# Optimization experiments

Hardware: AMD Instinct MI355X
Metric: run time of the kernel (lower is better)

Reference implementation:

```python
import jax, jax.numpy as jnp
import numpy as np
from jax import lax

NIC = 3            # image channels (immutable)
NC = 20            # total channels
FIRE_RATE = 0.5


def _sobel_kernel(nc):
    # depthwise kernel OIHW: for each channel, [sobel_x, sobel_y]
    sx = jnp.array([[-1., 0., 1.], [-2., 0., 2.], [-1., 0., 1.]], jnp.float32) / 8.0
    sy = sx.T
    k = jnp.stack([sx, sy], 0)[None]              # [1, 2, 3, 3]
    k = jnp.tile(k, (nc, 1, 1, 1)).reshape(2 * nc, 1, 3, 3)
    return k


def _perceive(x, sobel_k):
    # reflect padding as in filter_padding='reflect'
    xp = jnp.pad(x, ((0, 0), (0, 0), (1, 1), (1, 1)), mode='reflect')
    grad = lax.conv_general_dilated(
        xp, sobel_k, window_strides=(1, 1), padding='VALID',
        dimension_numbers=('NCHW', 'OIHW', 'NCHW'),
        feature_group_count=x.shape[1])
    # identity + 2 filters -> [B, 3*NC, H, W]
    return jnp.concatenate([x, grad], axis=1)


def reference(x, W1, b1, W2, steps):
    B, C, H, W = x.shape
    sobel_k = _sobel_kernel(C)
    # mask that zeroes dx on immutable image channels
    chan_mask = jnp.concatenate([jnp.zeros((NIC,), x.dtype),
                                 jnp.ones((C - NIC,), x.dtype)])[None, :, None, None]
    base_key = jax.random.key(42)

    def step_fn(xc, step):
        p = _perceive(xc, sobel_k)                                  # [B,3C,H,W]
        h = jax.nn.relu(jnp.einsum('bchw,kc->bkhw', p, W1) + b1[None, :, None, None])
        dx = jnp.einsum('bkhw,ck->bchw', h, W2)                      # [B,C,H,W]
        key = jax.random.fold_in(base_key, step)
        S = (jax.random.uniform(key, (B, 1, H, W)) < FIRE_RATE).astype(xc.dtype)
        dx = dx * S * chan_mask
        return xc + dx, None

    x, _ = lax.scan(step_fn, x, jnp.arange(steps))
    return x


def setup_inputs() -> dict:
    key = jax.random.key(0)
    k1, k2, k3 = jax.random.split(key, 3)
    x = jax.random.normal(k1, (8, NC, 256, 256), jnp.float32)
    W1 = jax.random.normal(k2, (128, 3 * NC), jnp.float32) * (1.0 / np.sqrt(3 * NC))
    b1 = jnp.zeros((128,), jnp.float32)
    # last layer is near-zero initialized in NCA practice; keep small for stability over 64 steps
    W2 = jax.random.normal(k3, (NC, 128), jnp.float32) * 0.01
    return {"x": x, "W1": W1, "b1": b1, "W2": W2, "steps": 64}
```

## Files before the change

kernel.cpp:

```cpp
#include <hip/hip_runtime.h>
#include <stdint.h>
#include <stddef.h>

#define HH 256
#define WW 256
#define NCH 20
#define KH 128

__host__ __device__ inline void tf2x32(uint32_t k0, uint32_t k1,
                                       uint32_t x0, uint32_t x1,
                                       uint32_t* o0, uint32_t* o1) {
  uint32_t ks0 = k0, ks1 = k1, ks2 = k0 ^ k1 ^ 0x1BD11BDAu;
  x0 += ks0; x1 += ks1;
#define RND(r) { x0 += x1; x1 = (x1 << (r)) | (x1 >> (32 - (r))); x1 ^= x0; }
  RND(13) RND(15) RND(26) RND(6)   x0 += ks1; x1 += ks2 + 1u;
  RND(17) RND(29) RND(16) RND(24)  x0 += ks2; x1 += ks0 + 2u;
  RND(13) RND(15) RND(26) RND(6)   x0 += ks0; x1 += ks1 + 3u;
  RND(17) RND(29) RND(16) RND(24)  x0 += ks1; x1 += ks2 + 4u;
  RND(13) RND(15) RND(26) RND(6)   x0 += ks2; x1 += ks0 + 5u;
#undef RND
  *o0 = x0; *o1 = x1;
}

__global__ __launch_bounds__(256) void nca_step(
    const float* __restrict__ xin, float* __restrict__ xout,
    const float* __restrict__ W1, const float* __restrict__ b1,
    const float* __restrict__ W2, uint32_t fk0, uint32_t fk1)
{
  __shared__ float xs[NCH][18][18];

  const int tid = threadIdx.x;
  const int bx = blockIdx.x, by = blockIdx.y, bb = blockIdx.z;
  const int x0t = bx << 4, y0t = by << 4;
  const float* xb = xin + (size_t)bb * (NCH * HH * WW);

  for (int idx = tid; idx < NCH * 18 * 18; idx += 256) {
    int c  = idx / 324;
    int r  = idx - c * 324;
    int ly = r / 18;
    int lx = r - ly * 18;
    int gy = y0t + ly - 1;
    int gx = x0t + lx - 1;
    gy = (gy < 0) ? -gy : gy;  gy = (gy >= HH) ? (2 * HH - 2 - gy) : gy;
    gx = (gx < 0) ? -gx : gx;  gx = (gx >= WW) ? (2 * WW - 2 - gx) : gx;
    xs[c][ly][lx] = xb[c * (HH * WW) + gy * WW + gx];
  }
  __syncthreads();

  const int tx = tid & 15, ty = tid >> 4;

  float p[3 * NCH];
#pragma unroll
  for (int c = 0; c < NCH; ++c) {
    float a00 = xs[c][ty    ][tx    ], a01 = xs[c][ty    ][tx + 1], a02 = xs[c][ty    ][tx + 2];
    float a10 = xs[c][ty + 1][tx    ], a11 = xs[c][ty + 1][tx + 1], a12 = xs[c][ty + 1][tx + 2];
    float a20 = xs[c][ty + 2][tx    ], a21 = xs[c][ty + 2][tx + 1], a22 = xs[c][ty + 2][tx + 2];
    p[c] = a11;
    p[NCH + 2 * c    ] = ((a02 - a00) + 2.f * (a12 - a10) + (a22 - a20)) * 0.125f;
    p[NCH + 2 * c + 1] = ((a20 - a00) + 2.f * (a21 - a01) + (a22 - a02)) * 0.125f;
  }

  float dxv[NCH];
#pragma unroll
  for (int c = 0; c < NCH; ++c) dxv[c] = 0.f;

  for (int k = 0; k < KH; ++k) {
    const float* w1r = W1 + k * 60;
    float h0 = b1[k], h1 = 0.f, h2 = 0.f, h3 = 0.f;
#pragma unroll
    for (int c = 0; c < 60; c += 4) {
      h0 = fmaf(w1r[c    ], p[c    ], h0);
      h1 = fmaf(w1r[c + 1], p[c + 1], h1);
      h2 = fmaf(w1r[c + 2], p[c + 2], h2);
      h3 = fmaf(w1r[c + 3], p[c + 3], h3);
    }
    float hk = fmaxf((h0 + h1) + (h2 + h3), 0.f);
#pragma unroll
    for (int c = 0; c < NCH; ++c)
      dxv[c] = fmaf(W2[c * KH + k], hk, dxv[c]);
  }

  uint32_t f = ((uint32_t)bb << 16) | ((uint32_t)(y0t + ty) << 8) | (uint32_t)(x0t + tx);
  uint32_t o0, o1;
  tf2x32(fk0, fk1, 0u, f, &o0, &o1);
  uint32_t bits = o0 ^ o1;
  float u = __uint_as_float((bits >> 9) | 0x3f800000u) - 1.0f;
  float fire = (u < 0.5f) ? 1.0f : 0.0f;

  size_t obase = (size_t)bb * (NCH * HH * WW) + (size_t)(y0t + ty) * WW + (x0t + tx);
#pragma unroll
  for (int c = 0; c < NCH; ++c) {
    float v = p[c];
    if (c >= 3) v = v + dxv[c] * fire;
    xout[obase + c * (HH * WW)] = v;
  }
}

extern "C" void kernel_launch(void* const* d_in, const int* in_sizes, int n_in,
                              void* d_out, int out_size, void* d_ws, size_t ws_size,
                              hipStream_t stream) {
  const float* x  = (const float*)d_in[0];
  const float* W1 = (const float*)d_in[1];
  const float* b1 = (const float*)d_in[2];
  const float* W2 = (const float*)d_in[3];
  const int steps = 64;

  float* bufWs  = (float*)d_ws;
  float* bufOut = (float*)d_out;

  dim3 grid(WW / 16, HH / 16, 8);
  dim3 block(256);

  const float* src = x;
  for (int s = 0; s < steps; ++s) {
    uint32_t fk0, fk1;
    tf2x32(0u, 42u, 0u, (uint32_t)s, &fk0, &fk1);
    float* dst = ((steps - 1 - s) & 1) ? bufWs : bufOut;
    nca_step<<<grid, block, 0, stream>>>(src, dst, W1, b1, W2, fk0, fk1);
    src = dst;
  }
}
```

Before: 13.24 ms.

## Compute two vertically adjacent pixels per thread and stage W2/b1 in LDS

Each thread now handles two vertically adjacent pixels on a 16x32 tile, so every W1 weight load feeds two sets of FMAs and the halo overhead per pixel shrinks. W2 and b1 are copied into shared memory once per block and read as float4 vectors, and the k loop is kept rolled. The goal is to cut the scalar and global weight-load traffic per FMA in this compute-bound MLP. In exchange, register use roughly doubles and the launch bound asks for 2 blocks per CU, which could force spills, and the grid has half as many blocks.

```diff
diff --git a/kernel.cpp b/kernel.cpp
--- a/kernel.cpp
+++ b/kernel.cpp
@@ -6,6 +6,10 @@
 #define WW 256
 #define NCH 20
 #define KH 128
+#define TSX 16
+#define TSY 32
+#define HALO_W 18
+#define HALO_H 34
 
 __host__ __device__ inline void tf2x32(uint32_t k0, uint32_t k1,
                                        uint32_t x0, uint32_t x1,
@@ -22,77 +26,114 @@
   *o0 = x0; *o1 = x1;
 }
 
-__global__ __launch_bounds__(256) void nca_step(
+__device__ inline float fire_of(uint32_t fk0, uint32_t fk1, uint32_t f) {
+  uint32_t o0, o1;
+  tf2x32(fk0, fk1, 0u, f, &o0, &o1);
+  uint32_t bits = o0 ^ o1;
+  float u = __uint_as_float((bits >> 9) | 0x3f800000u) - 1.0f;
+  return (u < 0.5f) ? 1.0f : 0.0f;
+}
+
+__global__ __launch_bounds__(256, 2) void nca_step(
     const float* __restrict__ xin, float* __restrict__ xout,
     const float* __restrict__ W1, const float* __restrict__ b1,
     const float* __restrict__ W2, uint32_t fk0, uint32_t fk1)
 {
-  __shared__ float xs[NCH][18][18];
+  __shared__ float xs[NCH][HALO_H][HALO_W];
+  __shared__ float w2b[KH][24];
 
   const int tid = threadIdx.x;
   const int bx = blockIdx.x, by = blockIdx.y, bb = blockIdx.z;
-  const int x0t = bx << 4, y0t = by << 4;
+  const int x0t = bx * TSX, y0t = by * TSY;
   const float* xb = xin + (size_t)bb * (NCH * HH * WW);
 
-  for (int idx = tid; idx < NCH * 18 * 18; idx += 256) {
-    int c  = idx / 324;
-    int r  = idx - c * 324;
-    int ly = r / 18;
-    int lx = r - ly * 18;
+  for (int idx = tid; idx < NCH * HALO_H * HALO_W; idx += 256) {
+    int c  = idx / (HALO_H * HALO_W);
+    int r  = idx - c * (HALO_H * HALO_W);
+    int ly = r / HALO_W;
+    int lx = r - ly * HALO_W;
     int gy = y0t + ly - 1;
     int gx = x0t + lx - 1;
     gy = (gy < 0) ? -gy : gy;  gy = (gy >= HH) ? (2 * HH - 2 - gy) : gy;
     gx = (gx < 0) ? -gx : gx;  gx = (gx >= WW) ? (2 * WW - 2 - gx) : gx;
     xs[c][ly][lx] = xb[c * (HH * WW) + gy * WW + gx];
   }
+  for (int idx = tid; idx < KH * 21; idx += 256) {
+    int k = idx / 21, c = idx - k * 21;
+    w2b[k][c] = (c < 20) ? W2[c * KH + k] : b1[k];
+  }
   __syncthreads();
 
-  const int tx = tid & 15, ty = tid >> 4;
+  const int tx = tid & 15, tyy = tid >> 4;
+  const int r0 = 2 * tyy;
 
-  float p[3 * NCH];
+  float pA[60], pB[60];
 #pragma unroll
   for (int c = 0; c < NCH; ++c) {
-    float a00 = xs[c][ty    ][tx    ], a01 = xs[c][ty    ][tx + 1], a02 = xs[c][ty    ][tx + 2];
-    float a10 = xs[c][ty + 1][tx    ], a11 = xs[c][ty + 1][tx + 1], a12 = xs[c][ty + 1][tx + 2];
-    float a20 = xs[c][ty + 2][tx    ], a21 = xs[c][ty + 2][tx + 1], a22 = xs[c][ty + 2][tx + 2];
-    p[c] = a11;
-    p[NCH + 2 * c    ] = ((a02 - a00) + 2.f * (a12 - a10) + (a22 - a20)) * 0.125f;
-    p[NCH + 2 * c + 1] = ((a20 - a00) + 2.f * (a21 - a01) + (a22 - a02)) * 0.125f;
+    float t00 = xs[c][r0    ][tx], t01 = xs[c][r0    ][tx + 1], t02 = xs[c][r0    ][tx + 2];
+    float t10 = xs[c][r0 + 1][tx], t11 = xs[c][r0 + 1][tx + 1], t12 = xs[c][r0 + 1][tx + 2];
+    float t20 = xs[c][r0 + 2][tx], t21 = xs[c][r0 + 2][tx + 1], t22 = xs[c][r0 + 2][tx + 2];
+    float t30 = xs[c][r0 + 3][tx], t31 = xs[c][r0 + 3][tx + 1], t32 = xs[c][r0 + 3][tx + 2];
+    pA[c] = t11;
+    pB[c] = t21;
+    pA[NCH + 2 * c    ] = ((t02 - t00) + 2.f * (t12 - t10) + (t22 - t20)) * 0.125f;
+    pA[NCH + 2 * c + 1] = ((t20 - t00) + 2.f * (t21 - t01) + (t22 - t02)) * 0.125f;
+    pB[NCH + 2 * c    ] = ((t12 - t10) + 2.f * (t22 - t20) + (t32 - t30)) * 0.125f;
+    pB[NCH + 2 * c + 1] = ((t30 - t10) + 2.f * (t31 - t11) + (t32 - t12)) * 0.125f;
   }
 
-  float dxv[NCH];
+  float dxA[NCH], dxB[NCH];
 #pragma unroll
-  for (int c = 0; c < NCH; ++c) dxv[c] = 0.f;
+  for (int c = 0; c < NCH; ++c) { dxA[c] = 0.f; dxB[c] = 0.f; }
 
+#pragma unroll 1
   for (int k = 0; k < KH; ++k) {
     const float* w1r = W1 + k * 60;
-    float h0 = b1[k], h1 = 0.f, h2 = 0.f, h3 = 0.f;
+    float4 wv0 = *(const float4*)&w2b[k][0];
+    float4 wv1 = *(const float4*)&w2b[k][4];
+    float4 wv2 = *(const float4*)&w2b[k][8];
+    float4 wv3 = *(const float4*)&w2b[k][12];
+    float4 wv4 = *(const float4*)&w2b[k][16];
+    float  bk  = w2b[k][20];
+
+    float a0 = bk, a1 = 0.f, a2 = 0.f, a3 = 0.f;
+    float c0 = bk, c1 = 0.f, c2 = 0.f, c3 = 0.f;
 #pragma unroll
     for (int c = 0; c < 60; c += 4) {
-      h0 = fmaf(w1r[c    ], p[c    ], h0);
-      h1 = fmaf(w1r[c + 1], p[c + 1], h1);
-      h2 = fmaf(w1r[c + 2], p[c + 2], h2);
-      h3 = fmaf(w1r[c + 3], p[c + 3], h3);
+      float w0 = w1r[c], w1v = w1r[c + 1], w2v = w1r[c + 2], w3v = w1r[c + 3];
+      a0 = fmaf(w0,  pA[c    ], a0);
+      a1 = fmaf(w1v, pA[c + 1], a1);
+      a2 = fmaf(w2v, pA[c + 2], a2);
+      a3 = fmaf(w3v, pA[c + 3], a3);
+      c0 = fmaf(w0,  pB[c    ], c0);
+      c1 = fmaf(w1v, pB[c + 1], c1);
+      c2 = fmaf(w2v, pB[c + 2], c2);
+      c3 = fmaf(w3v, pB[c + 3], c3);
     }
-    float hk = fmaxf((h0 + h1) + (h2 + h3), 0.f);
+    float hA = fmaxf((a0 + a1) + (a2 + a3), 0.f);
+    float hB = fmaxf((c0 + c1) + (c2 + c3), 0.f);
+
+    float w2arr[20] = { wv0.x, wv0.y, wv0.z, wv0.w,  wv1.x, wv1.y, wv1.z, wv1.w,
+                        wv2.x, wv2.y, wv2.z, wv2.w,  wv3.x, wv3.y, wv3.z, wv3.w,
+                        wv4.x, wv4.y, wv4.z, wv4.w };
 #pragma unroll
-    for (int c = 0; c < NCH; ++c)
-      dxv[c] = fmaf(W2[c * KH + k], hk, dxv[c]);
+    for (int c = 0; c < NCH; ++c) {
+      dxA[c] = fmaf(w2arr[c], hA, dxA[c]);
+      dxB[c] = fmaf(w2arr[c], hB, dxB[c]);
+    }
   }
 
-  uint32_t f = ((uint32_t)bb << 16) | ((uint32_t)(y0t + ty) << 8) | (uint32_t)(x0t + tx);
-  uint32_t o0, o1;
-  tf2x32(fk0, fk1, 0u, f, &o0, &o1);
-  uint32_t bits = o0 ^ o1;
-  float u = __uint_as_float((bits >> 9) | 0x3f800000u) - 1.0f;
-  float fire = (u < 0.5f) ? 1.0f : 0.0f;
+  const int gyA = y0t + r0, gyB = gyA + 1, gx = x0t + tx;
+  float fireA = fire_of(fk0, fk1, ((uint32_t)bb << 16) | ((uint32_t)gyA << 8) | (uint32_t)gx);
+  float fireB = fire_of(fk0, fk1, ((uint32_t)bb << 16) | ((uint32_t)gyB << 8) | (uint32_t)gx);
 
-  size_t obase = (size_t)bb * (NCH * HH * WW) + (size_t)(y0t + ty) * WW + (x0t + tx);
+  size_t baseA = (size_t)bb * (NCH * HH * WW) + (size_t)gyA * WW + gx;
 #pragma unroll
   for (int c = 0; c < NCH; ++c) {
-    float v = p[c];
-    if (c >= 3) v = v + dxv[c] * fire;
-    xout[obase + c * (HH * WW)] = v;
+    float vA = pA[c], vB = pB[c];
+    if (c >= 3) { vA = vA + dxA[c] * fireA; vB = vB + dxB[c] * fireB; }
+    xout[baseA + (size_t)c * (HH * WW)]      = vA;
+    xout[baseA + (size_t)c * (HH * WW) + WW] = vB;
   }
 }
 
@@ -108,7 +149,7 @@
   float* bufWs  = (float*)d_ws;
   float* bufOut = (float*)d_out;
 
-  dim3 grid(WW / 16, HH / 16, 8);
+  dim3 grid(WW / TSX, HH / TSY, 8);
   dim3 block(256);
 
   const float* src = x;
```

Measured after the change: 12.48 ms. -5.7%, faster.
